# Kernel tuning notes

Measured on AMD Instinct MI355X. Metric: run time of the kernel, lower is better.

## Reference

```python
import jax, jax.numpy as jnp
import numpy as np

N_NODES = 50000
N_EDGES = 800000
IN_CH = 128
HID = 128
NUM_GRAPHS = 512
BN_EPS = 1e-5


def setup_inputs() -> dict:
    key = jax.random.key(0)
    ks = jax.random.split(key, 16)
    x = jax.random.normal(ks[0], (N_NODES, IN_CH), dtype=jnp.float32)
    edge_index = jax.random.randint(ks[1], (2, N_EDGES), 0, N_NODES, dtype=jnp.int64)
    batch = jnp.sort(jax.random.randint(ks[2], (N_NODES,), 0, NUM_GRAPHS, dtype=jnp.int64))

    def glorot(k, shape):
        fan_in = shape[1]
        return jax.random.normal(k, shape, dtype=jnp.float32) / jnp.sqrt(jnp.float32(fan_in))

    # SAGEConv1: lin_l (aggr path, with bias), lin_r (root path, no bias)
    W1l = glorot(ks[3], (HID, IN_CH)); b1 = jnp.zeros((HID,), jnp.float32)
    W1r = glorot(ks[4], (HID, IN_CH))
    # SAGEConv2
    W2l = glorot(ks[5], (HID, HID)); b2 = jnp.zeros((HID,), jnp.float32)
    W2r = glorot(ks[6], (HID, HID))
    # MLP tail
    lin1_w = glorot(ks[7], (HID, HID)); lin1_b = jnp.zeros((HID,), jnp.float32)
    lin2_w = glorot(ks[8], (2, HID)); lin2_b = jnp.zeros((2,), jnp.float32)
    # BatchNorm1d (eval mode, running stats)
    gamma = jnp.ones((HID,), jnp.float32)
    beta = jnp.zeros((HID,), jnp.float32)
    running_mean = jax.random.normal(ks[9], (HID,), dtype=jnp.float32) * 0.1
    running_var = jax.random.uniform(ks[10], (HID,), dtype=jnp.float32, minval=0.5, maxval=1.5)
    return {
        "x": x, "edge_index": edge_index, "batch": batch,
        "W1l": W1l, "b1": b1, "W1r": W1r,
        "W2l": W2l, "b2": b2, "W2r": W2r,
        "lin1_w": lin1_w, "lin1_b": lin1_b,
        "lin2_w": lin2_w, "lin2_b": lin2_b,
        "gamma": gamma, "beta": beta,
        "running_mean": running_mean, "running_var": running_var,
    }


def _sage_conv(x, src, dst, Wl, bl, Wr):
    # mean-aggregate neighbor features (message flows src -> dst)
    n = x.shape[0]
    agg = jax.ops.segment_sum(x[src], dst, num_segments=n)  # [N, d]
    cnt = jax.ops.segment_sum(jnp.ones((src.shape[0], 1), x.dtype), dst, num_segments=n)
    mean = agg / jnp.maximum(cnt, 1.0)
    return mean @ Wl.T + bl + x @ Wr.T


def reference(x, edge_index, batch, W1l, b1, W1r, W2l, b2, W2r,
              lin1_w, lin1_b, lin2_w, lin2_b, gamma, beta,
              running_mean, running_var):
    src, dst = edge_index[0], edge_index[1]
    h = _sage_conv(x, src, dst, W1l, b1, W1r)      # [N, HID]
    h = _sage_conv(h, src, dst, W2l, b2, W2r)      # [N, HID]
    h = jax.ops.segment_sum(h, batch, num_segments=NUM_GRAPHS)  # global_add_pool -> [G, HID]
    h = h @ lin1_w.T + lin1_b
    # BatchNorm1d in eval mode (running stats)
    h = (h - running_mean) * jax.lax.rsqrt(running_var + BN_EPS) * gamma + beta
    h = jax.nn.relu(h)
    h = h @ lin2_w.T + lin2_b                      # [G, 2]
    # Dropout is identity in eval mode
    return h
```

## Files before the change

kernel.cpp:

```cpp
#include <hip/hip_runtime.h>
#include <hip/hip_bf16.h>

#define NN 50000
#define NE 800000
#define HID 128
#define NG 512
#define BN_EPS 1e-5f

typedef __attribute__((ext_vector_type(8))) short bf16x8;
typedef __attribute__((ext_vector_type(4))) float f32x4;

__device__ __forceinline__ ushort f2bf(float f) {
    uint u = __float_as_uint(f);
    uint r = (u + 0x7fffu + ((u >> 16) & 1u)) >> 16;
    return (ushort)r;
}
__device__ __forceinline__ float bf_lo(uint v) { return __uint_as_float(v << 16); }
__device__ __forceinline__ float bf_hi(uint v) { return __uint_as_float(v & 0xffff0000u); }

#define HIST_BLOCKS 782
#define CONV_BLOCKS 6250
#define WPREP_BLOCKS 32
#define POOLZ_BLOCKS 64
#define PH_GRID (HIST_BLOCKS + CONV_BLOCKS + WPREP_BLOCKS + POOLZ_BLOCKS)

__global__ __launch_bounds__(256) void prep_hist_kernel(const int* __restrict__ ei,
                                                        int* __restrict__ deg,
                                                        int* __restrict__ rank,
                                                        const float* __restrict__ x,
                                                        ushort* __restrict__ xb,
                                                        const float* __restrict__ W0,
                                                        const float* __restrict__ W1,
                                                        const float* __restrict__ W2,
                                                        const float* __restrict__ W3,
                                                        ushort* __restrict__ Wp,
                                                        float* __restrict__ pooled) {
    uint b = blockIdx.x;
    if (b < HIST_BLOCKS) {
        int e4 = b * 256 + threadIdx.x;
        if (e4 < NE / 4) {
            int4 dst = ((const int4*)(ei + NE))[e4];
            int4 rk;
            rk.x = atomicAdd(&deg[dst.x], 1);
            rk.y = atomicAdd(&deg[dst.y], 1);
            rk.z = atomicAdd(&deg[dst.z], 1);
            rk.w = atomicAdd(&deg[dst.w], 1);
            ((int4*)rank)[e4] = rk;
        }
    } else if (b < HIST_BLOCKS + CONV_BLOCKS) {
        int i = (b - HIST_BLOCKS) * 256 + threadIdx.x;
        float4 v = ((const float4*)x)[i];
        ushort4 o;
        o.x = f2bf(v.x);
        o.y = f2bf(v.y);
        o.z = f2bf(v.z);
        o.w = f2bf(v.w);
        ((ushort4*)xb)[i] = o;
    } else if (b < HIST_BLOCKS + CONV_BLOCKS + WPREP_BLOCKS) {
        int wu = (b - HIST_BLOCKS - CONV_BLOCKS) * 4 + (threadIdx.x >> 6);
        if (wu >= 128) return;
        int lane = threadIdx.x & 63;
        int m = wu >> 5;
        int g = wu & 31;
        int tile = g >> 2;
        int chunk = g & 3;
        const float* W = (m == 0) ? W0 : (m == 1) ? W1 : (m == 2) ? W2 : W3;
        int col = tile * 16 + (lane & 15);
        int k0 = chunk * 32 + (lane >> 4) * 8;
        ushort* dst = Wp + ((size_t)wu * 64 + lane) * 8;
#pragma unroll
        for (int j = 0; j < 8; ++j) dst[j] = f2bf(W[col * HID + k0 + j]);
    } else {
        int i = (b - HIST_BLOCKS - CONV_BLOCKS - WPREP_BLOCKS) * 256 + threadIdx.x;
        ((float4*)pooled)[i] = make_float4(0.f, 0.f, 0.f, 0.f);
    }
}

__global__ __launch_bounds__(256) void scan1_kernel(const int* __restrict__ deg,
                                                    int* __restrict__ row_start,
                                                    int* __restrict__ bsums, int n) {
    __shared__ int wsum[4];
    int i = blockIdx.x * 256 + threadIdx.x;
    int lane = threadIdx.x & 63;
    int wid = threadIdx.x >> 6;
    int v = (i < n) ? deg[i] : 0;
    int sc = v;
#pragma unroll
    for (int off = 1; off < 64; off <<= 1) {
        int t = __shfl_up(sc, off);
        if (lane >= off) sc += t;
    }
    if (lane == 63) wsum[wid] = sc;
    __syncthreads();
    int wpre = 0;
#pragma unroll
    for (int k = 0; k < 4; ++k) wpre += (k < wid) ? wsum[k] : 0;
    if (i < n) row_start[i] = wpre + sc - v;
    if (threadIdx.x == 255) bsums[blockIdx.x] = wpre + sc;
}

__global__ __launch_bounds__(256) void scan23_kernel(int* __restrict__ row_start,
                                                     const int* __restrict__ bsums, int n) {
    __shared__ int sred[4];
    int v = (threadIdx.x < blockIdx.x) ? bsums[threadIdx.x] : 0;
#pragma unroll
    for (int off = 32; off > 0; off >>= 1) v += __shfl_xor(v, off);
    if ((threadIdx.x & 63) == 0) sred[threadIdx.x >> 6] = v;
    __syncthreads();
    int total = sred[0] + sred[1] + sred[2] + sred[3];
    int i = blockIdx.x * 256 + threadIdx.x;
    if (i < n) row_start[i] += total;
}

__global__ __launch_bounds__(256) void fill_kernel(const int* __restrict__ ei,
                                                   const int* __restrict__ row_start,
                                                   const int* __restrict__ rank,
                                                   int* __restrict__ srclist) {
    int e4 = blockIdx.x * 256 + threadIdx.x;
    if (e4 >= NE / 4) return;
    int4 src = ((const int4*)ei)[e4];
    int4 dst = ((const int4*)(ei + NE))[e4];
    int4 rk = ((const int4*)rank)[e4];
    int p0 = row_start[dst.x] + rk.x;
    int p1 = row_start[dst.y] + rk.y;
    int p2 = row_start[dst.z] + rk.z;
    int p3 = row_start[dst.w] + rk.w;
    srclist[p0] = src.x;
    srclist[p1] = src.y;
    srclist[p2] = src.z;
    srclist[p3] = src.w;
}

__global__ __launch_bounds__(256) void aggregate_kernel(const ushort* __restrict__ feat,
                                                        const int* __restrict__ row_start,
                                                        const int* __restrict__ deg,
                                                        const int* __restrict__ srclist,
                                                        ushort* __restrict__ mean, int n) {
    int node = blockIdx.x * 4 + (threadIdx.x >> 6);
    if (node >= n) return;
    int lane = threadIdx.x & 63;
    int cl = lane & 15;
    int sub = lane >> 4;
    const uint4* fb = (const uint4*)feat;
    int s0 = row_start[node];
    int d = deg[node];

    float a[8];
#pragma unroll
    for (int i = 0; i < 8; ++i) a[i] = 0.f;

    int j = 0;
    for (; j + 16 <= d; j += 16) {
        int i0 = srclist[s0 + j + sub];
        int i1 = srclist[s0 + j + 4 + sub];
        int i2 = srclist[s0 + j + 8 + sub];
        int i3 = srclist[s0 + j + 12 + sub];
        uint4 v0 = fb[(size_t)i0 * 16 + cl];
        uint4 v1 = fb[(size_t)i1 * 16 + cl];
        uint4 v2 = fb[(size_t)i2 * 16 + cl];
        uint4 v3 = fb[(size_t)i3 * 16 + cl];
        a[0] += (bf_lo(v0.x) + bf_lo(v1.x)) + (bf_lo(v2.x) + bf_lo(v3.x));
        a[1] += (bf_hi(v0.x) + bf_hi(v1.x)) + (bf_hi(v2.x) + bf_hi(v3.x));
        a[2] += (bf_lo(v0.y) + bf_lo(v1.y)) + (bf_lo(v2.y) + bf_lo(v3.y));
        a[3] += (bf_hi(v0.y) + bf_hi(v1.y)) + (bf_hi(v2.y) + bf_hi(v3.y));
        a[4] += (bf_lo(v0.z) + bf_lo(v1.z)) + (bf_lo(v2.z) + bf_lo(v3.z));
        a[5] += (bf_hi(v0.z) + bf_hi(v1.z)) + (bf_hi(v2.z) + bf_hi(v3.z));
        a[6] += (bf_lo(v0.w) + bf_lo(v1.w)) + (bf_lo(v2.w) + bf_lo(v3.w));
        a[7] += (bf_hi(v0.w) + bf_hi(v1.w)) + (bf_hi(v2.w) + bf_hi(v3.w));
    }
    if (j < d) {
        int dm1 = d - 1;
        int k0 = j + sub;
        int k1 = j + 4 + sub;
        int k2 = j + 8 + sub;
        int k3 = j + 12 + sub;
        int i0 = srclist[s0 + min(k0, dm1)];
        int i1 = srclist[s0 + min(k1, dm1)];
        int i2 = srclist[s0 + min(k2, dm1)];
        int i3 = srclist[s0 + min(k3, dm1)];
        uint4 v0 = fb[(size_t)i0 * 16 + cl];
        uint4 v1 = fb[(size_t)i1 * 16 + cl];
        uint4 v2 = fb[(size_t)i2 * 16 + cl];
        uint4 v3 = fb[(size_t)i3 * 16 + cl];
        float m0 = (k0 < d) ? 1.f : 0.f;
        float m1 = (k1 < d) ? 1.f : 0.f;
        float m2 = (k2 < d) ? 1.f : 0.f;
        float m3 = (k3 < d) ? 1.f : 0.f;
        a[0] += m0 * bf_lo(v0.x) + m1 * bf_lo(v1.x) + m2 * bf_lo(v2.x) + m3 * bf_lo(v3.x);
        a[1] += m0 * bf_hi(v0.x) + m1 * bf_hi(v1.x) + m2 * bf_hi(v2.x) + m3 * bf_hi(v3.x);
        a[2] += m0 * bf_lo(v0.y) + m1 * bf_lo(v1.y) + m2 * bf_lo(v2.y) + m3 * bf_lo(v3.y);
        a[3] += m0 * bf_hi(v0.y) + m1 * bf_hi(v1.y) + m2 * bf_hi(v2.y) + m3 * bf_hi(v3.y);
        a[4] += m0 * bf_lo(v0.z) + m1 * bf_lo(v1.z) + m2 * bf_lo(v2.z) + m3 * bf_lo(v3.z);
        a[5] += m0 * bf_hi(v0.z) + m1 * bf_hi(v1.z) + m2 * bf_hi(v2.z) + m3 * bf_hi(v3.z);
        a[6] += m0 * bf_lo(v0.w) + m1 * bf_lo(v1.w) + m2 * bf_lo(v2.w) + m3 * bf_lo(v3.w);
        a[7] += m0 * bf_hi(v0.w) + m1 * bf_hi(v1.w) + m2 * bf_hi(v2.w) + m3 * bf_hi(v3.w);
    }

#pragma unroll
    for (int i = 0; i < 8; ++i) {
        float v = a[i];
        v += __shfl_xor(v, 16);
        v += __shfl_xor(v, 32);
        a[i] = v;
    }

    if (sub == 0) {
        float inv = 1.0f / fmaxf((float)d, 1.0f);
        uint4 o;
        o.x = (uint)f2bf(a[0] * inv) | ((uint)f2bf(a[1] * inv) << 16);
        o.y = (uint)f2bf(a[2] * inv) | ((uint)f2bf(a[3] * inv) << 16);
        o.z = (uint)f2bf(a[4] * inv) | ((uint)f2bf(a[5] * inv) << 16);
        o.w = (uint)f2bf(a[6] * inv) | ((uint)f2bf(a[7] * inv) << 16);
        ((uint4*)mean)[(size_t)node * 16 + cl] = o;
    }
}

template <bool POOL>
__global__ __launch_bounds__(256) void sage_gemm_mfma(const ushort* __restrict__ Amean,
                                                      const ushort* __restrict__ Aroot,
                                                      const ushort* __restrict__ WpL,
                                                      const float* __restrict__ bias,
                                                      const int* __restrict__ batch,
                                                      void* __restrict__ outv, int nwaves) {
    int w = blockIdx.x * 4 + (threadIdx.x >> 6);
    if (w >= nwaves) return;
    int lane = threadIdx.x & 63;
    int mrow = lane & 15;
    int quad = lane >> 4;
    int r0 = w * 16;

    f32x4 acc[8];
#pragma unroll
    for (int t = 0; t < 8; ++t) acc[t] = (f32x4){0.f, 0.f, 0.f, 0.f};

    const ushort* arow_m = Amean + ((size_t)(r0 + mrow)) * HID + quad * 8;
    const ushort* arow_r = Aroot + ((size_t)(r0 + mrow)) * HID + quad * 8;

#pragma unroll
    for (int half = 0; half < 2; ++half) {
        const ushort* arow = half ? arow_r : arow_m;
        const ushort* wb = WpL + (size_t)half * 16384 + (size_t)lane * 8;
#pragma unroll
        for (int c = 0; c < 4; ++c) {
            bf16x8 a = *(const bf16x8*)(arow + c * 32);
#pragma unroll
            for (int t = 0; t < 8; ++t) {
                bf16x8 b = *(const bf16x8*)(wb + (size_t)(t * 4 + c) * 512);
                acc[t] = __builtin_amdgcn_mfma_f32_16x16x32_bf16(a, b, acc[t], 0, 0, 0);
            }
        }
    }

    if (POOL) {
        float* pooled = (float*)outv;
        int rbase = r0 + quad * 4;
        int g0 = batch[rbase + 0];
        int g1 = batch[rbase + 1];
        int g2 = batch[rbase + 2];
        int g3 = batch[rbase + 3];
#pragma unroll
        for (int t = 0; t < 8; ++t) {
            int col = t * 16 + mrow;
            float bv = bias[col];
            float v0 = acc[t][0] + bv;
            float v1 = acc[t][1] + bv;
            float v2 = acc[t][2] + bv;
            float v3 = acc[t][3] + bv;
            int cg = g0;
            float s = v0;
            if (g1 == cg) s += v1; else { atomicAdd(&pooled[(size_t)cg * HID + col], s); cg = g1; s = v1; }
            if (g2 == cg) s += v2; else { atomicAdd(&pooled[(size_t)cg * HID + col], s); cg = g2; s = v2; }
            if (g3 == cg) s += v3; else { atomicAdd(&pooled[(size_t)cg * HID + col], s); cg = g3; s = v3; }
            atomicAdd(&pooled[(size_t)cg * HID + col], s);
        }
    } else {
        ushort* out = (ushort*)outv;
#pragma unroll
        for (int t = 0; t < 8; ++t) {
            int col = t * 16 + mrow;
            float bv = bias[col];
#pragma unroll
            for (int r = 0; r < 4; ++r) {
                int row = r0 + quad * 4 + r;
                out[(size_t)row * HID + col] = f2bf(acc[t][r] + bv);
            }
        }
    }
}

__global__ __launch_bounds__(128) void tail_kernel(const float* __restrict__ pooled,
                                                   const float* __restrict__ lin1_w,
                                                   const float* __restrict__ lin1_b,
                                                   const float* __restrict__ lin2_w,
                                                   const float* __restrict__ lin2_b,
                                                   const float* __restrict__ gamma,
                                                   const float* __restrict__ beta,
                                                   const float* __restrict__ rmean,
                                                   const float* __restrict__ rvar,
                                                   float* __restrict__ out) {
    __shared__ float Wt[64 * 128];
    __shared__ float p[128];
    __shared__ float tbuf[128];
    int g = blockIdx.x;
    int c = threadIdx.x;
    p[c] = pooled[g * HID + c];
    float acc = lin1_b[c];
    int kk = c & 63;
    int chalf = c >> 6;
    for (int k0 = 0; k0 < 128; k0 += 64) {
        __syncthreads();
        for (int i = 0; i < 64; ++i) {
            int crow = i * 2 + chalf;
            float v = lin1_w[crow * HID + k0 + kk];
            Wt[kk * 128 + (crow ^ (kk & 31))] = v;
        }
        __syncthreads();
#pragma unroll
        for (int k = 0; k < 64; ++k) {
            acc += p[k0 + k] * Wt[k * 128 + (c ^ (k & 31))];
        }
    }
    float v = (acc - rmean[c]) * rsqrtf(rvar[c] + BN_EPS) * gamma[c] + beta[c];
    v = fmaxf(v, 0.f);
    tbuf[c] = v;
    __syncthreads();
    int j = c >> 6;
    int lane = c & 63;
    float partial = tbuf[lane] * lin2_w[j * HID + lane] +
                    tbuf[lane + 64] * lin2_w[j * HID + lane + 64];
    for (int off = 32; off > 0; off >>= 1) partial += __shfl_down(partial, off);
    if (lane == 0) out[g * 2 + j] = partial + lin2_b[j];
}

extern "C" void kernel_launch(void* const* d_in, const int* in_sizes, int n_in,
                              void* d_out, int out_size, void* d_ws, size_t ws_size,
                              hipStream_t stream) {
    const float* x = (const float*)d_in[0];
    const int* ei = (const int*)d_in[1];
    const int* batch = (const int*)d_in[2];
    const float* W1l = (const float*)d_in[3];
    const float* b1 = (const float*)d_in[4];
    const float* W1r = (const float*)d_in[5];
    const float* W2l = (const float*)d_in[6];
    const float* b2 = (const float*)d_in[7];
    const float* W2r = (const float*)d_in[8];
    const float* lin1_w = (const float*)d_in[9];
    const float* lin1_b = (const float*)d_in[10];
    const float* lin2_w = (const float*)d_in[11];
    const float* lin2_b = (const float*)d_in[12];
    const float* gamma = (const float*)d_in[13];
    const float* beta = (const float*)d_in[14];
    const float* rmean = (const float*)d_in[15];
    const float* rvar = (const float*)d_in[16];
    float* out = (float*)d_out;

    const int N = NN, E = NE;
    const int NWAVES = N / 16;

    char* p = (char*)d_ws;
    auto carve = [&](size_t bytes) {
        void* r = (void*)p;
        p += (bytes + 255) & ~(size_t)255;
        return r;
    };
    int* deg = (int*)carve((size_t)N * 4);
    int* row_start = (int*)carve((size_t)N * 4);
    int* bsums = (int*)carve(1024 * 4);
    int* rank = (int*)carve((size_t)E * 4);
    int* srclist = (int*)carve((size_t)E * 4 + 64);
    ushort* xb = (ushort*)carve((size_t)N * HID * 2);
    ushort* meanb = (ushort*)carve((size_t)N * HID * 2);
    ushort* h1 = (ushort*)carve((size_t)N * HID * 2);
    float* pooled = (float*)carve((size_t)NG * HID * 4);
    ushort* Wp = (ushort*)carve(4 * 32 * 64 * 8 * 2);

    hipMemsetAsync(deg, 0, (size_t)N * 4, stream);

    prep_hist_kernel<<<PH_GRID, 256, 0, stream>>>(ei, deg, rank, x, xb,
                                                  W1l, W1r, W2l, W2r, Wp, pooled);

    const int scanBlocks = (N + 255) / 256;
    scan1_kernel<<<scanBlocks, 256, 0, stream>>>(deg, row_start, bsums, N);
    scan23_kernel<<<scanBlocks, 256, 0, stream>>>(row_start, bsums, N);
    fill_kernel<<<(E / 4 + 255) / 256, 256, 0, stream>>>(ei, row_start, rank, srclist);

    aggregate_kernel<<<(N + 3) / 4, 256, 0, stream>>>(xb, row_start, deg, srclist, meanb, N);
    sage_gemm_mfma<false><<<(NWAVES + 3) / 4, 256, 0, stream>>>(meanb, xb, Wp, b1, nullptr, h1,
                                                                NWAVES);
    aggregate_kernel<<<(N + 3) / 4, 256, 0, stream>>>(h1, row_start, deg, srclist, meanb, N);
    sage_gemm_mfma<true><<<(NWAVES + 3) / 4, 256, 0, stream>>>(meanb, h1, Wp + 32768, b2, batch,
                                                               pooled, NWAVES);
    tail_kernel<<<NG, 128, 0, stream>>>(pooled, lin1_w, lin1_b, lin2_w, lin2_b,
                                        gamma, beta, rmean, rvar, out);
}
```

Measured before the change: 261.2 us.

## Remap neighbor aggregation to one node per 4 lanes with channel slices across blocks

```diff
diff --git a/kernel.cpp b/kernel.cpp
--- a/kernel.cpp
+++ b/kernel.cpp
@@ -131,88 +131,59 @@
     srclist[p3] = src.w;
 }
 
+#define AGG_SLICES 4
 __global__ __launch_bounds__(256) void aggregate_kernel(const ushort* __restrict__ feat,
                                                         const int* __restrict__ row_start,
                                                         const int* __restrict__ deg,
                                                         const int* __restrict__ srclist,
                                                         ushort* __restrict__ mean, int n) {
-    int node = blockIdx.x * 4 + (threadIdx.x >> 6);
+    int slice = blockIdx.x & (AGG_SLICES - 1);
+    int nb = blockIdx.x >> 2;
+    int wave = threadIdx.x >> 6;
+    int lane = threadIdx.x & 63;
+    int slot = lane >> 2;
+    int cl = lane & 3;
+    int node = (nb * 4 + wave) * 16 + slot;
     if (node >= n) return;
-    int lane = threadIdx.x & 63;
-    int cl = lane & 15;
-    int sub = lane >> 4;
-    const uint4* fb = (const uint4*)feat;
     int s0 = row_start[node];
     int d = deg[node];
+    const uint4* fb = (const uint4*)feat;
+    int coff = slice * 4 + cl;
 
     float a[8];
 #pragma unroll
     for (int i = 0; i < 8; ++i) a[i] = 0.f;
 
-    int j = 0;
-    for (; j + 16 <= d; j += 16) {
-        int i0 = srclist[s0 + j + sub];
-        int i1 = srclist[s0 + j + 4 + sub];
-        int i2 = srclist[s0 + j + 8 + sub];
-        int i3 = srclist[s0 + j + 12 + sub];
-        uint4 v0 = fb[(size_t)i0 * 16 + cl];
-        uint4 v1 = fb[(size_t)i1 * 16 + cl];
-        uint4 v2 = fb[(size_t)i2 * 16 + cl];
-        uint4 v3 = fb[(size_t)i3 * 16 + cl];
-        a[0] += (bf_lo(v0.x) + bf_lo(v1.x)) + (bf_lo(v2.x) + bf_lo(v3.x));
-        a[1] += (bf_hi(v0.x) + bf_hi(v1.x)) + (bf_hi(v2.x) + bf_hi(v3.x));
-        a[2] += (bf_lo(v0.y) + bf_lo(v1.y)) + (bf_lo(v2.y) + bf_lo(v3.y));
-        a[3] += (bf_hi(v0.y) + bf_hi(v1.y)) + (bf_hi(v2.y) + bf_hi(v3.y));
-        a[4] += (bf_lo(v0.z) + bf_lo(v1.z)) + (bf_lo(v2.z) + bf_lo(v3.z));
-        a[5] += (bf_hi(v0.z) + bf_hi(v1.z)) + (bf_hi(v2.z) + bf_hi(v3.z));
-        a[6] += (bf_lo(v0.w) + bf_lo(v1.w)) + (bf_lo(v2.w) + bf_lo(v3.w));
-        a[7] += (bf_hi(v0.w) + bf_hi(v1.w)) + (bf_hi(v2.w) + bf_hi(v3.w));
-    }
-    if (j < d) {
-        int dm1 = d - 1;
-        int k0 = j + sub;
-        int k1 = j + 4 + sub;
-        int k2 = j + 8 + sub;
-        int k3 = j + 12 + sub;
-        int i0 = srclist[s0 + min(k0, dm1)];
-        int i1 = srclist[s0 + min(k1, dm1)];
-        int i2 = srclist[s0 + min(k2, dm1)];
-        int i3 = srclist[s0 + min(k3, dm1)];
-        uint4 v0 = fb[(size_t)i0 * 16 + cl];
-        uint4 v1 = fb[(size_t)i1 * 16 + cl];
-        uint4 v2 = fb[(size_t)i2 * 16 + cl];
-        uint4 v3 = fb[(size_t)i3 * 16 + cl];
-        float m0 = (k0 < d) ? 1.f : 0.f;
-        float m1 = (k1 < d) ? 1.f : 0.f;
-        float m2 = (k2 < d) ? 1.f : 0.f;
-        float m3 = (k3 < d) ? 1.f : 0.f;
-        a[0] += m0 * bf_lo(v0.x) + m1 * bf_lo(v1.x) + m2 * bf_lo(v2.x) + m3 * bf_lo(v3.x);
-        a[1] += m0 * bf_hi(v0.x) + m1 * bf_hi(v1.x) + m2 * bf_hi(v2.x) + m3 * bf_hi(v3.x);
-        a[2] += m0 * bf_lo(v0.y) + m1 * bf_lo(v1.y) + m2 * bf_lo(v2.y) + m3 * bf_lo(v3.y);
-        a[3] += m0 * bf_hi(v0.y) + m1 * bf_hi(v1.y) + m2 * bf_hi(v2.y) + m3 * bf_hi(v3.y);
-        a[4] += m0 * bf_lo(v0.z) + m1 * bf_lo(v1.z) + m2 * bf_lo(v2.z) + m3 * bf_lo(v3.z);
-        a[5] += m0 * bf_hi(v0.z) + m1 * bf_hi(v1.z) + m2 * bf_hi(v2.z) + m3 * bf_hi(v3.z);
-        a[6] += m0 * bf_lo(v0.w) + m1 * bf_lo(v1.w) + m2 * bf_lo(v2.w) + m3 * bf_lo(v3.w);
-        a[7] += m0 * bf_hi(v0.w) + m1 * bf_hi(v1.w) + m2 * bf_hi(v2.w) + m3 * bf_hi(v3.w);
-    }
-
-#pragma unroll
-    for (int i = 0; i < 8; ++i) {
-        float v = a[i];
-        v += __shfl_xor(v, 16);
-        v += __shfl_xor(v, 32);
-        a[i] = v;
-    }
-
-    if (sub == 0) {
-        float inv = 1.0f / fmaxf((float)d, 1.0f);
-        uint4 o;
-        o.x = (uint)f2bf(a[0] * inv) | ((uint)f2bf(a[1] * inv) << 16);
-        o.y = (uint)f2bf(a[2] * inv) | ((uint)f2bf(a[3] * inv) << 16);
-        o.z = (uint)f2bf(a[4] * inv) | ((uint)f2bf(a[5] * inv) << 16);
-        o.w = (uint)f2bf(a[6] * inv) | ((uint)f2bf(a[7] * inv) << 16);
-        ((uint4*)mean)[(size_t)node * 16 + cl] = o;
-    }
+    int dm1 = d - 1;
+    for (int j = 0; j < d; j += 4) {
+        int i0 = __builtin_nontemporal_load(srclist + s0 + j);
+        int i1 = __builtin_nontemporal_load(srclist + s0 + min(j + 1, dm1));
+        int i2 = __builtin_nontemporal_load(srclist + s0 + min(j + 2, dm1));
+        int i3 = __builtin_nontemporal_load(srclist + s0 + min(j + 3, dm1));
+        uint4 v0 = fb[(size_t)i0 * 16 + coff];
+        uint4 v1 = fb[(size_t)i1 * 16 + coff];
+        uint4 v2 = fb[(size_t)i2 * 16 + coff];
+        uint4 v3 = fb[(size_t)i3 * 16 + coff];
+        float m1 = (j + 1 < d) ? 1.f : 0.f;
+        float m2 = (j + 2 < d) ? 1.f : 0.f;
+        float m3 = (j + 3 < d) ? 1.f : 0.f;
+        a[0] += bf_lo(v0.x) + m1 * bf_lo(v1.x) + m2 * bf_lo(v2.x) + m3 * bf_lo(v3.x);
+        a[1] += bf_hi(v0.x) + m1 * bf_hi(v1.x) + m2 * bf_hi(v2.x) + m3 * bf_hi(v3.x);
+        a[2] += bf_lo(v0.y) + m1 * bf_lo(v1.y) + m2 * bf_lo(v2.y) + m3 * bf_lo(v3.y);
+        a[3] += bf_hi(v0.y) + m1 * bf_hi(v1.y) + m2 * bf_hi(v2.y) + m3 * bf_hi(v3.y);
+        a[4] += bf_lo(v0.z) + m1 * bf_lo(v1.z) + m2 * bf_lo(v2.z) + m3 * bf_lo(v3.z);
+        a[5] += bf_hi(v0.z) + m1 * bf_hi(v1.z) + m2 * bf_hi(v2.z) + m3 * bf_hi(v3.z);
+        a[6] += bf_lo(v0.w) + m1 * bf_lo(v1.w) + m2 * bf_lo(v2.w) + m3 * bf_lo(v3.w);
+        a[7] += bf_hi(v0.w) + m1 * bf_hi(v1.w) + m2 * bf_hi(v2.w) + m3 * bf_hi(v3.w);
+    }
+
+    float inv = 1.0f / fmaxf((float)d, 1.0f);
+    uint4 o;
+    o.x = (uint)f2bf(a[0] * inv) | ((uint)f2bf(a[1] * inv) << 16);
+    o.y = (uint)f2bf(a[2] * inv) | ((uint)f2bf(a[3] * inv) << 16);
+    o.z = (uint)f2bf(a[4] * inv) | ((uint)f2bf(a[5] * inv) << 16);
+    o.w = (uint)f2bf(a[6] * inv) | ((uint)f2bf(a[7] * inv) << 16);
+    ((uint4*)mean)[(size_t)node * 16 + coff] = o;
 }
 
 template <bool POOL>
@@ -384,10 +355,11 @@
     scan23_kernel<<<scanBlocks, 256, 0, stream>>>(row_start, bsums, N);
     fill_kernel<<<(E / 4 + 255) / 256, 256, 0, stream>>>(ei, row_start, rank, srclist);
 
-    aggregate_kernel<<<(N + 3) / 4, 256, 0, stream>>>(xb, row_start, deg, srclist, meanb, N);
+    const int aggBlocks = AGG_SLICES * ((N + 63) / 64);
+    aggregate_kernel<<<aggBlocks, 256, 0, stream>>>(xb, row_start, deg, srclist, meanb, N);
     sage_gemm_mfma<false><<<(NWAVES + 3) / 4, 256, 0, stream>>>(meanb, xb, Wp, b1, nullptr, h1,
                                                                 NWAVES);
-    aggregate_kernel<<<(N + 3) / 4, 256, 0, stream>>>(h1, row_start, deg, srclist, meanb, N);
+    aggregate_kernel<<<aggBlocks, 256, 0, stream>>>(h1, row_start, deg, srclist, meanb, N);
     sage_gemm_mfma<true><<<(NWAVES + 3) / 4, 256, 0, stream>>>(meanb, h1, Wp + 32768, b2, batch,
                                                                pooled, NWAVES);
     tail_kernel<<<NG, 128, 0, stream>>>(pooled, lin1_w, lin1_b, lin2_w, lin2_b,
```

Measured after the change: 315.0 us. 1.21x slower.

## Apply layer-1 linear transforms before aggregation and fuse root add into aggregate

Applied to the files above, without the earlier changes.

```diff
diff --git a/kernel.cpp b/kernel.cpp
--- a/kernel.cpp
+++ b/kernel.cpp
@@ -18,21 +18,34 @@
 __device__ __forceinline__ float bf_lo(uint v) { return __uint_as_float(v << 16); }
 __device__ __forceinline__ float bf_hi(uint v) { return __uint_as_float(v & 0xffff0000u); }
 
+__device__ __forceinline__ bf16x8 ld_frag_f32(const float* __restrict__ p) {
+    float4 f0 = *(const float4*)p;
+    float4 f1 = *(const float4*)(p + 4);
+    bf16x8 r;
+    r[0] = (short)f2bf(f0.x); r[1] = (short)f2bf(f0.y);
+    r[2] = (short)f2bf(f0.z); r[3] = (short)f2bf(f0.w);
+    r[4] = (short)f2bf(f1.x); r[5] = (short)f2bf(f1.y);
+    r[6] = (short)f2bf(f1.z); r[7] = (short)f2bf(f1.w);
+    return r;
+}
+
 #define HIST_BLOCKS 782
-#define CONV_BLOCKS 6250
-#define WPREP_BLOCKS 32
+#define GEMM1_BLOCKS 782
+#define WPREP_BLOCKS 16
 #define POOLZ_BLOCKS 64
-#define PH_GRID (HIST_BLOCKS + CONV_BLOCKS + WPREP_BLOCKS + POOLZ_BLOCKS)
+#define PH_GRID (HIST_BLOCKS + GEMM1_BLOCKS + WPREP_BLOCKS + POOLZ_BLOCKS)
 
 __global__ __launch_bounds__(256) void prep_hist_kernel(const int* __restrict__ ei,
                                                         int* __restrict__ deg,
                                                         int* __restrict__ rank,
                                                         const float* __restrict__ x,
-                                                        ushort* __restrict__ xb,
-                                                        const float* __restrict__ W0,
-                                                        const float* __restrict__ W1,
-                                                        const float* __restrict__ W2,
-                                                        const float* __restrict__ W3,
+                                                        const float* __restrict__ W1l,
+                                                        const float* __restrict__ W1r,
+                                                        const float* __restrict__ b1,
+                                                        ushort* __restrict__ y1,
+                                                        ushort* __restrict__ r1,
+                                                        const float* __restrict__ W2l,
+                                                        const float* __restrict__ W2r,
                                                         ushort* __restrict__ Wp,
                                                         float* __restrict__ pooled) {
     uint b = blockIdx.x;
@@ -47,31 +60,61 @@
             rk.w = atomicAdd(&deg[dst.w], 1);
             ((int4*)rank)[e4] = rk;
         }
-    } else if (b < HIST_BLOCKS + CONV_BLOCKS) {
-        int i = (b - HIST_BLOCKS) * 256 + threadIdx.x;
-        float4 v = ((const float4*)x)[i];
-        ushort4 o;
-        o.x = f2bf(v.x);
-        o.y = f2bf(v.y);
-        o.z = f2bf(v.z);
-        o.w = f2bf(v.w);
-        ((ushort4*)xb)[i] = o;
-    } else if (b < HIST_BLOCKS + CONV_BLOCKS + WPREP_BLOCKS) {
-        int wu = (b - HIST_BLOCKS - CONV_BLOCKS) * 4 + (threadIdx.x >> 6);
-        if (wu >= 128) return;
+    } else if (b < HIST_BLOCKS + GEMM1_BLOCKS) {
+        int w = (b - HIST_BLOCKS) * 4 + (threadIdx.x >> 6);
+        if (w >= NN / 16) return;
+        int lane = threadIdx.x & 63;
+        int mrow = lane & 15;
+        int quad = lane >> 4;
+        int r0 = w * 16;
+
+        f32x4 accY[8], accR[8];
+#pragma unroll
+        for (int t = 0; t < 8; ++t) {
+            accY[t] = (f32x4){0.f, 0.f, 0.f, 0.f};
+            accR[t] = (f32x4){0.f, 0.f, 0.f, 0.f};
+        }
+        const float* xrow = x + (size_t)(r0 + mrow) * HID + quad * 8;
+#pragma unroll
+        for (int c = 0; c < 4; ++c) {
+            bf16x8 a = ld_frag_f32(xrow + c * 32);
+#pragma unroll
+            for (int t = 0; t < 8; ++t) {
+                const float* wbase = (size_t)(t * 16 + mrow) * HID + c * 32 + quad * 8 + (float*)0;
+                bf16x8 bl = ld_frag_f32(W1l + (size_t)(t * 16 + mrow) * HID + c * 32 + quad * 8);
+                accY[t] = __builtin_amdgcn_mfma_f32_16x16x32_bf16(a, bl, accY[t], 0, 0, 0);
+                bf16x8 br = ld_frag_f32(W1r + (size_t)(t * 16 + mrow) * HID + c * 32 + quad * 8);
+                accR[t] = __builtin_amdgcn_mfma_f32_16x16x32_bf16(a, br, accR[t], 0, 0, 0);
+                (void)wbase;
+            }
+        }
+#pragma unroll
+        for (int t = 0; t < 8; ++t) {
+            int col = t * 16 + mrow;
+            float bv = b1[col];
+#pragma unroll
+            for (int r = 0; r < 4; ++r) {
+                int row = r0 + quad * 4 + r;
+                y1[(size_t)row * HID + col] = f2bf(accY[t][r]);
+                r1[(size_t)row * HID + col] = f2bf(accR[t][r] + bv);
+            }
+        }
+    } else if (b < HIST_BLOCKS + GEMM1_BLOCKS + WPREP_BLOCKS) {
+        int wu = (b - HIST_BLOCKS - GEMM1_BLOCKS) * 4 + (threadIdx.x >> 6);
+        if (wu >= 64) return;
         int lane = threadIdx.x & 63;
         int m = wu >> 5;
         int g = wu & 31;
         int tile = g >> 2;
         int chunk = g & 3;
-        const float* W = (m == 0) ? W0 : (m == 1) ? W1 : (m == 2) ? W2 : W3;
+        const float* W = (m == 0) ? W2l : W2r;
         int col = tile * 16 + (lane & 15);
         int k0 = chunk * 32 + (lane >> 4) * 8;
         ushort* dst = Wp + ((size_t)wu * 64 + lane) * 8;
 #pragma unroll
         for (int j = 0; j < 8; ++j) dst[j] = f2bf(W[col * HID + k0 + j]);
     } else {
-        int i = (b - HIST_BLOCKS - CONV_BLOCKS - WPREP_BLOCKS) * 256 + threadIdx.x;
+        int i = (b - HIST_BLOCKS - GEMM1_BLOCKS - WPREP_BLOCKS) * 256 + threadIdx.x;
         ((float4*)pooled)[i] = make_float4(0.f, 0.f, 0.f, 0.f);
     }
 }
@@ -131,11 +174,13 @@
     srclist[p3] = src.w;
 }
 
+template <bool ADD_R>
 __global__ __launch_bounds__(256) void aggregate_kernel(const ushort* __restrict__ feat,
                                                         const int* __restrict__ row_start,
                                                         const int* __restrict__ deg,
                                                         const int* __restrict__ srclist,
-                                                        ushort* __restrict__ mean, int n) {
+                                                        const ushort* __restrict__ rres,
+                                                        ushort* __restrict__ outbuf, int n) {
     int node = blockIdx.x * 4 + (threadIdx.x >> 6);
     if (node >= n) return;
     int lane = threadIdx.x & 63;
@@ -206,22 +251,31 @@
 
     if (sub == 0) {
         float inv = 1.0f / fmaxf((float)d, 1.0f);
+        float h[8];
+#pragma unroll
+        for (int i = 0; i < 8; ++i) h[i] = a[i] * inv;
+        if (ADD_R) {
+            uint4 rv = ((const uint4*)rres)[(size_t)node * 16 + cl];
+            h[0] += bf_lo(rv.x); h[1] += bf_hi(rv.x);
+            h[2] += bf_lo(rv.y); h[3] += bf_hi(rv.y);
+            h[4] += bf_lo(rv.z); h[5] += bf_hi(rv.z);
+            h[6] += bf_lo(rv.w); h[7] += bf_hi(rv.w);
+        }
         uint4 o;
-        o.x = (uint)f2bf(a[0] * inv) | ((uint)f2bf(a[1] * inv) << 16);
-        o.y = (uint)f2bf(a[2] * inv) | ((uint)f2bf(a[3] * inv) << 16);
-        o.z = (uint)f2bf(a[4] * inv) | ((uint)f2bf(a[5] * inv) << 16);
-        o.w = (uint)f2bf(a[6] * inv) | ((uint)f2bf(a[7] * inv) << 16);
-        ((uint4*)mean)[(size_t)node * 16 + cl] = o;
-    }
-}
-
-template <bool POOL>
-__global__ __launch_bounds__(256) void sage_gemm_mfma(const ushort* __restrict__ Amean,
+        o.x = (uint)f2bf(h[0]) | ((uint)f2bf(h[1]) << 16);
+        o.y = (uint)f2bf(h[2]) | ((uint)f2bf(h[3]) << 16);
+        o.z = (uint)f2bf(h[4]) | ((uint)f2bf(h[5]) << 16);
+        o.w = (uint)f2bf(h[6]) | ((uint)f2bf(h[7]) << 16);
+        ((uint4*)outbuf)[(size_t)node * 16 + cl] = o;
+    }
+}
+
+__global__ __launch_bounds__(256) void sage_gemm_pool(const ushort* __restrict__ Amean,
                                                       const ushort* __restrict__ Aroot,
                                                       const ushort* __restrict__ WpL,
                                                       const float* __restrict__ bias,
                                                       const int* __restrict__ batch,
-                                                      void* __restrict__ outv, int nwaves) {
+                                                      float* __restrict__ pooled, int nwaves) {
     int w = blockIdx.x * 4 + (threadIdx.x >> 6);
     if (w >= nwaves) return;
     int lane = threadIdx.x & 63;
@@ -251,40 +305,25 @@
         }
     }
 
-    if (POOL) {
-        float* pooled = (float*)outv;
-        int rbase = r0 + quad * 4;
-        int g0 = batch[rbase + 0];
-        int g1 = batch[rbase + 1];
-        int g2 = batch[rbase + 2];
-        int g3 = batch[rbase + 3];
-#pragma unroll
-        for (int t = 0; t < 8; ++t) {
-            int col = t * 16 + mrow;
-            float bv = bias[col];
-            float v0 = acc[t][0] + bv;
-            float v1 = acc[t][1] + bv;
-            float v2 = acc[t][2] + bv;
-            float v3 = acc[t][3] + bv;
-            int cg = g0;
-            float s = v0;
-            if (g1 == cg) s += v1; else { atomicAdd(&pooled[(size_t)cg * HID + col], s); cg = g1; s = v1; }
-            if (g2 == cg) s += v2; else { atomicAdd(&pooled[(size_t)cg * HID + col], s); cg = g2; s = v2; }
-            if (g3 == cg) s += v3; else { atomicAdd(&pooled[(size_t)cg * HID + col], s); cg = g3; s = v3; }
-            atomicAdd(&pooled[(size_t)cg * HID + col], s);
-        }
-    } else {
-        ushort* out = (ushort*)outv;
-#pragma unroll
-        for (int t = 0; t < 8; ++t) {
-            int col = t * 16 + mrow;
-            float bv = bias[col];
-#pragma unroll
-            for (int r = 0; r < 4; ++r) {
-                int row = r0 + quad * 4 + r;
-                out[(size_t)row * HID + col] = f2bf(acc[t][r] + bv);
-            }
-        }
+    int rbase = r0 + quad * 4;
+    int g0 = batch[rbase + 0];
+    int g1 = batch[rbase + 1];
+    int g2 = batch[rbase + 2];
+    int g3 = batch[rbase + 3];
+#pragma unroll
+    for (int t = 0; t < 8; ++t) {
+        int col = t * 16 + mrow;
+        float bv = bias[col];
+        float v0 = acc[t][0] + bv;
+        float v1 = acc[t][1] + bv;
+        float v2 = acc[t][2] + bv;
+        float v3 = acc[t][3] + bv;
+        int cg = g0;
+        float s = v0;
+        if (g1 == cg) s += v1; else { atomicAdd(&pooled[(size_t)cg * HID + col], s); cg = g1; s = v1; }
+        if (g2 == cg) s += v2; else { atomicAdd(&pooled[(size_t)cg * HID + col], s); cg = g2; s = v2; }
+        if (g3 == cg) s += v3; else { atomicAdd(&pooled[(size_t)cg * HID + col], s); cg = g3; s = v3; }
+        atomicAdd(&pooled[(size_t)cg * HID + col], s);
     }
 }
 
@@ -368,28 +407,29 @@
     int* bsums = (int*)carve(1024 * 4);
     int* rank = (int*)carve((size_t)E * 4);
     int* srclist = (int*)carve((size_t)E * 4 + 64);
-    ushort* xb = (ushort*)carve((size_t)N * HID * 2);
+    ushort* y1 = (ushort*)carve((size_t)N * HID * 2);
+    ushort* r1 = (ushort*)carve((size_t)N * HID * 2);
+    ushort* h1 = (ushort*)carve((size_t)N * HID * 2);
     ushort* meanb = (ushort*)carve((size_t)N * HID * 2);
-    ushort* h1 = (ushort*)carve((size_t)N * HID * 2);
     float* pooled = (float*)carve((size_t)NG * HID * 4);
-    ushort* Wp = (ushort*)carve(4 * 32 * 64 * 8 * 2);
+    ushort* Wp = (ushort*)carve(2 * 32 * 64 * 8 * 2);
 
     hipMemsetAsync(deg, 0, (size_t)N * 4, stream);
 
-    prep_hist_kernel<<<PH_GRID, 256, 0, stream>>>(ei, deg, rank, x, xb,
-                                                  W1l, W1r, W2l, W2r, Wp, pooled);
+    prep_hist_kernel<<<PH_GRID, 256, 0, stream>>>(ei, deg, rank, x, W1l, W1r, b1, y1, r1,
+                                                  W2l, W2r, Wp, pooled);
 
     const int scanBlocks = (N + 255) / 256;
     scan1_kernel<<<scanBlocks, 256, 0, stream>>>(deg, row_start, bsums, N);
     scan23_kernel<<<scanBlocks, 256, 0, stream>>>(row_start, bsums, N);
     fill_kernel<<<(E / 4 + 255) / 256, 256, 0, stream>>>(ei, row_start, rank, srclist);
 
-    aggregate_kernel<<<(N + 3) / 4, 256, 0, stream>>>(xb, row_start, deg, srclist, meanb, N);
-    sage_gemm_mfma<false><<<(NWAVES + 3) / 4, 256, 0, stream>>>(meanb, xb, Wp, b1, nullptr, h1,
-                                                                NWAVES);
-    aggregate_kernel<<<(N + 3) / 4, 256, 0, stream>>>(h1, row_start, deg, srclist, meanb, N);
-    sage_gemm_mfma<true><<<(NWAVES + 3) / 4, 256, 0, stream>>>(meanb, h1, Wp + 32768, b2, batch,
-                                                               pooled, NWAVES);
+    aggregate_kernel<true><<<(N + 3) / 4, 256, 0, stream>>>(y1, row_start, deg, srclist, r1,
+                                                            h1, N);
+    aggregate_kernel<false><<<(N + 3) / 4, 256, 0, stream>>>(h1, row_start, deg, srclist,
+                                                             nullptr, meanb, N);
+    sage_gemm_pool<<<(NWAVES + 3) / 4, 256, 0, stream>>>(meanb, h1, Wp, b2, batch, pooled,
+                                                         NWAVES);
     tail_kernel<<<NG, 128, 0, stream>>>(pooled, lin1_w, lin1_b, lin2_w, lin2_b,
                                         gamma, beta, rmean, rvar, out);
 }
```

After: 312.9 us. 19.8% more time.
